# Optimization experiments

Hardware: AMD Instinct MI355X
Metric: run time of the kernel (lower is better)

## Reference

```python
import jax, jax.numpy as jnp
import numpy as np

EPS = 1e-9
N_NODES = 100000
N_EDGES = 1600000
N_FEAT = 256


def _normalize(x):
    # ProjectiveUHG.normalize: scale each point to the unit sphere (projective rep)
    return x / (jnp.linalg.norm(x, axis=-1, keepdims=True) + EPS)


def _mink(a, b):
    # UHG bilinear form: Euclidean on first d-1 coords, minus on the last
    return jnp.sum(a[..., :-1] * b[..., :-1], axis=-1) - a[..., -1] * b[..., -1]


def _uhg_dist(a, b):
    # projective quadrance q = 1 - <a,b>^2 / (<a,a><b,b>); distance = sqrt(q)
    q = 1.0 - _mink(a, b) ** 2 / (_mink(a, a) * _mink(b, b) + EPS)
    return jnp.sqrt(jnp.clip(q, 0.0))


def _message_pass(h, row, col):
    # vectorized gather -> per-edge UHG distance -> exp weight -> scatter-add
    xs = h[row]                                    # [E, D]
    xt = h[col]                                    # [E, D]
    w = jnp.exp(-_uhg_dist(xs, xt))[:, None]       # [E, 1]
    return jax.ops.segment_sum(xs * w, col, num_segments=h.shape[0])


def setup_inputs() -> dict:
    key = jax.random.key(0)
    ks = jax.random.split(key, 12)
    s = 0.05
    return {
        "x": jax.random.normal(ks[0], (N_NODES, N_FEAT), jnp.float32),
        "edge_index": jax.random.randint(ks[1], (2, N_EDGES), 0, N_NODES, jnp.int64 if jax.config.jax_enable_x64 else jnp.int32),
        "W_in": jax.random.normal(ks[2], (N_FEAT, 128), jnp.float32) * s,
        "b_in": jnp.zeros((128,), jnp.float32),
        "W1": jax.random.normal(ks[3], (128, 128), jnp.float32) * s,
        "b1": jnp.zeros((128,), jnp.float32),
        "W2": jax.random.normal(ks[4], (128, 64), jnp.float32) * s,
        "b2": jnp.zeros((64,), jnp.float32),
        "Wc1": jax.random.normal(ks[5], (64, 32), jnp.float32) * s,
        "bc1": jnp.zeros((32,), jnp.float32),
        "Wc2": jax.random.normal(ks[6], (32, 1), jnp.float32) * s,
        "bc2": jnp.zeros((1,), jnp.float32),
    }


def reference(x, edge_index, W_in, b_in, W1, b1, W2, b2, Wc1, bc1, Wc2, bc2):
    row, col = edge_index[0], edge_index[1]
    h = _normalize(jax.nn.relu(x @ W_in + b_in))       # [N, 128]
    agg = _message_pass(h, row, col)                   # [N, 128]
    h = _normalize(jax.nn.relu(agg @ W1 + b1))         # [N, 128]
    agg = _message_pass(h, row, col)                   # [N, 128]
    h = _normalize(jax.nn.relu(agg @ W2 + b2))         # [N, 64]
    h = jax.nn.relu(h @ Wc1 + bc1)                     # dropout is eval-mode identity
    return jax.nn.sigmoid(h @ Wc2 + bc2)               # [N, 1]
```

## Files before the change

### kernel.cpp

```cpp
#include <hip/hip_runtime.h>
#include <hip/hip_bf16.h>
#include <math.h>


template<int K, int M, bool WANT_MQ>
__global__ __launch_bounds__(256) void gemm_tile_norm(
    const float* __restrict__ A, const float* __restrict__ W,
    const float* __restrict__ bias, float* __restrict__ H,
    float* __restrict__ mqout, int N)
{
    constexpr int BM  = 128;
    constexpr int KB  = 32;
    constexpr int NTX = M / 8;
    constexpr int NTY = 256 / NTX;
    constexpr int TR  = BM / NTY;
    constexpr int SA  = BM + 4;
    constexpr int SW  = M + 4;

    __shared__ float As[KB][SA];
    __shared__ float Ws[KB][SW];

    const int tid  = threadIdx.x;
    const int tx   = tid % NTX;
    const int ty   = tid / NTX;
    const int row0 = blockIdx.x * BM;

    float acc[TR][8];
    #pragma unroll
    for (int r = 0; r < TR; ++r)
        #pragma unroll
        for (int c = 0; c < 8; ++c) acc[r][c] = 0.f;

    const int sf4 = tid % 8;
    const int sr0 = tid / 8;

    for (int kc = 0; kc < K / KB; ++kc) {
        if (kc) __syncthreads();
        #pragma unroll
        for (int t = 0; t < 4; ++t) {
            const int r    = t * 32 + sr0;
            const int grow = row0 + r;
            float4 v = {0.f, 0.f, 0.f, 0.f};
            if (grow < N)
                v = *(const float4*)(A + (size_t)grow * K + kc * KB + sf4 * 4);
            As[sf4 * 4 + 0][r] = v.x;
            As[sf4 * 4 + 1][r] = v.y;
            As[sf4 * 4 + 2][r] = v.z;
            As[sf4 * 4 + 3][r] = v.w;
        }
        #pragma unroll
        for (int t = 0; t < KB * M / 4 / 256; ++t) {
            const int idx = t * 256 + tid;
            const int kk  = idx / (M / 4);
            const int c4  = idx % (M / 4);
            *(float4*)&Ws[kk][c4 * 4] =
                *(const float4*)(W + (size_t)(kc * KB + kk) * M + c4 * 4);
        }
        __syncthreads();

        #pragma unroll 8
        for (int k = 0; k < KB; ++k) {
            const float4 w0 = *(const float4*)&Ws[k][tx * 8];
            const float4 w1 = *(const float4*)&Ws[k][tx * 8 + 4];
            float a[TR];
            #pragma unroll
            for (int rq = 0; rq < TR / 4; ++rq) {
                const float4 av = *(const float4*)&As[k][ty * TR + rq * 4];
                a[rq * 4 + 0] = av.x; a[rq * 4 + 1] = av.y;
                a[rq * 4 + 2] = av.z; a[rq * 4 + 3] = av.w;
            }
            #pragma unroll
            for (int r = 0; r < TR; ++r) {
                acc[r][0] += a[r] * w0.x;
                acc[r][1] += a[r] * w0.y;
                acc[r][2] += a[r] * w0.z;
                acc[r][3] += a[r] * w0.w;
                acc[r][4] += a[r] * w1.x;
                acc[r][5] += a[r] * w1.y;
                acc[r][6] += a[r] * w1.z;
                acc[r][7] += a[r] * w1.w;
            }
        }
    }

    const float4 b0 = *(const float4*)(bias + tx * 8);
    const float4 b1 = *(const float4*)(bias + tx * 8 + 4);

    #pragma unroll
    for (int r = 0; r < TR; ++r) {
        float v[8];
        v[0] = fmaxf(acc[r][0] + b0.x, 0.f);
        v[1] = fmaxf(acc[r][1] + b0.y, 0.f);
        v[2] = fmaxf(acc[r][2] + b0.z, 0.f);
        v[3] = fmaxf(acc[r][3] + b0.w, 0.f);
        v[4] = fmaxf(acc[r][4] + b1.x, 0.f);
        v[5] = fmaxf(acc[r][5] + b1.y, 0.f);
        v[6] = fmaxf(acc[r][6] + b1.z, 0.f);
        v[7] = fmaxf(acc[r][7] + b1.w, 0.f);

        float ss = 0.f;
        #pragma unroll
        for (int c = 0; c < 8; ++c) ss += v[c] * v[c];
        #pragma unroll
        for (int off = 1; off < NTX; off <<= 1) ss += __shfl_xor(ss, off);

        const float inv = 1.f / (sqrtf(ss) + 1e-9f);
        const int row = row0 + ty * TR + r;
        if (row < N) {
            float4 o0 = {v[0] * inv, v[1] * inv, v[2] * inv, v[3] * inv};
            float4 o1 = {v[4] * inv, v[5] * inv, v[6] * inv, v[7] * inv};
            *(float4*)(H + (size_t)row * M + tx * 8)     = o0;
            *(float4*)(H + (size_t)row * M + tx * 8 + 4) = o1;
            if (WANT_MQ && tx == NTX - 1) {
                const float hl = v[7] * inv;
                mqout[row] = ss * inv * inv - 2.f * hl * hl;
            }
        }
    }
}


__global__ void hist_kernel(const int* __restrict__ col, int* __restrict__ cnt, int E) {
    const int i = blockIdx.x * blockDim.x + threadIdx.x;
    if (i < E) atomicAdd(&cnt[col[i]], 1);
}

#define SCAN_TPB 256
#define SCAN_VPT 4

__global__ void scan1_kernel(const int* __restrict__ cnt, int* __restrict__ base,
                             int* __restrict__ bsum, int N) {
    __shared__ int s[SCAN_TPB];
    const int t  = threadIdx.x;
    const int i0 = blockIdx.x * (SCAN_TPB * SCAN_VPT) + t * SCAN_VPT;
    int v[SCAN_VPT]; int tot = 0;
    #pragma unroll
    for (int j = 0; j < SCAN_VPT; ++j) {
        v[j] = (i0 + j < N) ? cnt[i0 + j] : 0;
        tot += v[j];
    }
    s[t] = tot;
    __syncthreads();
    for (int off = 1; off < SCAN_TPB; off <<= 1) {
        const int x = (t >= off) ? s[t - off] : 0;
        __syncthreads();
        s[t] += x;
        __syncthreads();
    }
    const int excl = s[t] - tot;
    if (t == SCAN_TPB - 1) bsum[blockIdx.x] = s[SCAN_TPB - 1];
    int run = excl;
    #pragma unroll
    for (int j = 0; j < SCAN_VPT; ++j) {
        if (i0 + j < N) base[i0 + j] = run;
        run += v[j];
    }
}

__global__ void scan2_kernel(int* __restrict__ bsum, int nb) {
    __shared__ int s[SCAN_TPB];
    const int t = threadIdx.x;
    const int v = (t < nb) ? bsum[t] : 0;
    s[t] = v;
    __syncthreads();
    for (int off = 1; off < SCAN_TPB; off <<= 1) {
        const int x = (t >= off) ? s[t - off] : 0;
        __syncthreads();
        s[t] += x;
        __syncthreads();
    }
    if (t < nb) bsum[t] = s[t] - v;
}

__global__ void scan3_kernel(int* __restrict__ base, const int* __restrict__ bsum,
                             int* __restrict__ cursor, int N) {
    const int i = blockIdx.x * blockDim.x + threadIdx.x;
    if (i < N) {
        const int v = base[i] + bsum[i / (SCAN_TPB * SCAN_VPT)];
        base[i]   = v;
        cursor[i] = v;
    }
}

__global__ void scatter_kernel(const int* __restrict__ row, const int* __restrict__ col,
                               int* __restrict__ cursor, int* __restrict__ srow, int E) {
    const int i = blockIdx.x * blockDim.x + threadIdx.x;
    if (i < E) {
        const int pos = atomicAdd(&cursor[col[i]], 1);
        srow[pos] = row[i];
    }
}

__global__ __launch_bounds__(256) void message_pass_csr8(
    const float* __restrict__ h, const float* __restrict__ mq,
    const int* __restrict__ srow, const int* __restrict__ base,
    const int* __restrict__ cnt, float* __restrict__ agg, int N)
{
    const int node = (int)((blockIdx.x * 256u + threadIdx.x) >> 6);
    if (node >= N) return;
    const int lane = threadIdx.x & 63;
    const int gl   = lane & 7;
    const int g    = lane >> 3;

    const float4* hb = (const float4*)(h + (size_t)node * 128 + gl * 16);
    const float4 b0 = hb[0];
    const float4 b1 = hb[1];
    const float4 b2 = hb[2];
    const float4 b3 = hb[3];
    const float mqc = mq[node];

    const int nb = cnt[node];
    const int st = base[node];

    float4 acc0 = {0.f,0.f,0.f,0.f}, acc1 = {0.f,0.f,0.f,0.f};
    float4 acc2 = {0.f,0.f,0.f,0.f}, acc3 = {0.f,0.f,0.f,0.f};

    const int iters = (nb + 7) >> 3;
    for (int t = 0; t < iters; ++t) {
        const int ei  = t * 8 + g;
        const bool act = ei < nb;
        const int e   = st + (act ? ei : 0);
        const int r   = srow[e];
        const float4* ha = (const float4*)(h + (size_t)r * 128 + gl * 16);
        const float4 a0 = ha[0];
        const float4 a1 = ha[1];
        const float4 a2 = ha[2];
        const float4 a3 = ha[3];
        const float mqr = mq[r];

        float p = a0.x*b0.x + a0.y*b0.y + a0.z*b0.z + a0.w*b0.w
                + a1.x*b1.x + a1.y*b1.y + a1.z*b1.z + a1.w*b1.w
                + a2.x*b2.x + a2.y*b2.y + a2.z*b2.z + a2.w*b2.w
                + a3.x*b3.x + a3.y*b3.y + a3.z*b3.z;
        p += (gl == 7) ? -a3.w * b3.w : a3.w * b3.w;
        p += __shfl_xor(p, 1);
        p += __shfl_xor(p, 2);
        p += __shfl_xor(p, 4);

        const float denom = mqr * mqc + 1e-9f;
        float q = 1.f - (p * p) / denom;
        q = fmaxf(q, 0.f);
        float w = expf(-sqrtf(q));
        w = act ? w : 0.f;

        acc0.x += a0.x*w; acc0.y += a0.y*w; acc0.z += a0.z*w; acc0.w += a0.w*w;
        acc1.x += a1.x*w; acc1.y += a1.y*w; acc1.z += a1.z*w; acc1.w += a1.w*w;
        acc2.x += a2.x*w; acc2.y += a2.y*w; acc2.z += a2.z*w; acc2.w += a2.w*w;
        acc3.x += a3.x*w; acc3.y += a3.y*w; acc3.z += a3.z*w; acc3.w += a3.w*w;
    }

    #pragma unroll
    for (int off = 8; off < 64; off <<= 1) {
        acc0.x += __shfl_xor(acc0.x, off); acc0.y += __shfl_xor(acc0.y, off);
        acc0.z += __shfl_xor(acc0.z, off); acc0.w += __shfl_xor(acc0.w, off);
        acc1.x += __shfl_xor(acc1.x, off); acc1.y += __shfl_xor(acc1.y, off);
        acc1.z += __shfl_xor(acc1.z, off); acc1.w += __shfl_xor(acc1.w, off);
        acc2.x += __shfl_xor(acc2.x, off); acc2.y += __shfl_xor(acc2.y, off);
        acc2.z += __shfl_xor(acc2.z, off); acc2.w += __shfl_xor(acc2.w, off);
        acc3.x += __shfl_xor(acc3.x, off); acc3.y += __shfl_xor(acc3.y, off);
        acc3.z += __shfl_xor(acc3.z, off); acc3.w += __shfl_xor(acc3.w, off);
    }
    if (g == 0) {
        float4* out = (float4*)(agg + (size_t)node * 128 + gl * 16);
        out[0] = acc0;
        out[1] = acc1;
        out[2] = acc2;
        out[3] = acc3;
    }
}

__global__ __launch_bounds__(256) void message_pass(
    const float* __restrict__ h, const float* __restrict__ mq,
    const int* __restrict__ row, const int* __restrict__ col,
    float* __restrict__ agg, int E)
{
    const int wid  = (int)((blockIdx.x * (unsigned)blockDim.x + threadIdx.x) >> 6);
    const int lane = threadIdx.x & 63;
    if (wid >= E) return;

    const int r = row[wid];
    const int c = col[wid];

    const float a0 = h[(size_t)r * 128 + lane];
    const float a1 = h[(size_t)r * 128 + 64 + lane];
    const float b0 = h[(size_t)c * 128 + lane];
    const float b1 = h[(size_t)c * 128 + 64 + lane];

    float p = a0 * b0 + ((lane == 63) ? -a1 * b1 : a1 * b1);
    #pragma unroll
    for (int off = 1; off < 64; off <<= 1) p += __shfl_xor(p, off);

    const float denom = mq[r] * mq[c] + 1e-9f;
    float q = 1.f - (p * p) / denom;
    q = fmaxf(q, 0.f);
    const float w = expf(-sqrtf(q));

    atomicAdd(&agg[(size_t)c * 128 + lane],      a0 * w);
    atomicAdd(&agg[(size_t)c * 128 + 64 + lane], a1 * w);
}

__global__ __launch_bounds__(256) void classifier_kernel(
    const float* __restrict__ h3, const float* __restrict__ Wc1,
    const float* __restrict__ bc1, const float* __restrict__ Wc2,
    const float* __restrict__ bc2, float* __restrict__ out, int N)
{
    __shared__ float w1[64 * 32];
    __shared__ float w2[32];
    __shared__ float b1s[32];

    const int tid = threadIdx.x;
    for (int i = tid; i < 64 * 32; i += 256) w1[i] = Wc1[i];
    if (tid < 32) { w2[tid] = Wc2[tid]; b1s[tid] = bc1[tid]; }
    __syncthreads();

    const int n = blockIdx.x * 256 + tid;
    if (n >= N) return;

    float t1[32];
    #pragma unroll
    for (int c = 0; c < 32; ++c) t1[c] = b1s[c];

    const float4* hrow = (const float4*)(h3 + (size_t)n * 64);
    #pragma unroll
    for (int k4 = 0; k4 < 16; ++k4) {
        const float4 hv = hrow[k4];
        const int k = k4 * 4;
        #pragma unroll
        for (int c = 0; c < 32; ++c) {
            t1[c] += hv.x * w1[(k + 0) * 32 + c] + hv.y * w1[(k + 1) * 32 + c]
                   + hv.z * w1[(k + 2) * 32 + c] + hv.w * w1[(k + 3) * 32 + c];
        }
    }

    float z = bc2[0];
    #pragma unroll
    for (int c = 0; c < 32; ++c) z += fmaxf(t1[c], 0.f) * w2[c];
    out[n] = 1.f / (1.f + expf(-z));
}

extern "C" void kernel_launch(void* const* d_in, const int* in_sizes, int n_in,
                              void* d_out, int out_size, void* d_ws, size_t ws_size,
                              hipStream_t stream)
{
    const float* x    = (const float*)d_in[0];
    const int*   ei   = (const int*)  d_in[1];
    const float* W_in = (const float*)d_in[2];
    const float* b_in = (const float*)d_in[3];
    const float* W1   = (const float*)d_in[4];
    const float* b1   = (const float*)d_in[5];
    const float* W2   = (const float*)d_in[6];
    const float* b2   = (const float*)d_in[7];
    const float* Wc1  = (const float*)d_in[8];
    const float* bc1  = (const float*)d_in[9];
    const float* Wc2  = (const float*)d_in[10];
    const float* bc2  = (const float*)d_in[11];
    float* out = (float*)d_out;

    const int N = in_sizes[0] / 256;
    const int E = in_sizes[1] / 2;
    const int* row = ei;
    const int* col = ei + E;

    float* bufA = (float*)d_ws;
    float* bufB = bufA + (size_t)N * 128;
    float* mq   = bufB + (size_t)N * 128;
    int*   cnt  = (int*)(mq + N);
    int*   base = cnt + N;
    int*   cur  = base + N;
    int*   bsum = cur + N;
    int*   srow = bsum + 256;

    const size_t need = ((size_t)N * 257 + (size_t)N * 3 + 256 + (size_t)E) * 4;
    const bool use_csr = ws_size >= need;

    const int scan_blk = (N + SCAN_TPB * SCAN_VPT - 1) / (SCAN_TPB * SCAN_VPT);

    if (use_csr) {
        hipMemsetAsync(cnt, 0, (size_t)N * sizeof(int), stream);
        hist_kernel<<<(E + 255) / 256, 256, 0, stream>>>(col, cnt, E);
        scan1_kernel<<<scan_blk, SCAN_TPB, 0, stream>>>(cnt, base, bsum, N);
        scan2_kernel<<<1, SCAN_TPB, 0, stream>>>(bsum, scan_blk);
        scan3_kernel<<<(N + 255) / 256, 256, 0, stream>>>(base, bsum, cur, N);
        scatter_kernel<<<(E + 255) / 256, 256, 0, stream>>>(row, col, cur, srow, E);
    }

    const int gemm_blk = (N + 127) / 128;
    const int mp_blocks_csr = (N + 3) / 4;
    const int mp_blocks_atm = (E + 3) / 4;

    gemm_tile_norm<256, 128, true><<<gemm_blk, 256, 0, stream>>>(x, W_in, b_in, bufA, mq, N);
    if (use_csr) {
        message_pass_csr8<<<mp_blocks_csr, 256, 0, stream>>>(bufA, mq, srow, base, cnt, bufB, N);
    } else {
        hipMemsetAsync(bufB, 0, (size_t)N * 128 * sizeof(float), stream);
        message_pass<<<mp_blocks_atm, 256, 0, stream>>>(bufA, mq, row, col, bufB, E);
    }

    gemm_tile_norm<128, 128, true><<<gemm_blk, 256, 0, stream>>>(bufB, W1, b1, bufA, mq, N);
    if (use_csr) {
        message_pass_csr8<<<mp_blocks_csr, 256, 0, stream>>>(bufA, mq, srow, base, cnt, bufB, N);
    } else {
        hipMemsetAsync(bufB, 0, (size_t)N * 128 * sizeof(float), stream);
        message_pass<<<mp_blocks_atm, 256, 0, stream>>>(bufA, mq, row, col, bufB, E);
    }

    gemm_tile_norm<128, 64, false><<<gemm_blk, 256, 0, stream>>>(bufB, W2, b2, bufA, nullptr, N);

    classifier_kernel<<<(N + 255) / 256, 256, 0, stream>>>(bufA, Wc1, bc1, Wc2, bc2, out, N);
}
```

Before: 787.3 us.

## Presort edges by row then column buckets before CSR scatter

Replaces the single random atomic scatter that builds the CSR source list with a two-pass bucket sort: edges are first partitioned by source-row bucket, then stably by destination-column bucket, and only then scattered per destination. The goal is to make the final per-column scatter and the later gathers of source rows more local, so that neighbour lists are roughly ordered by source row and cache hits improve. The cost is two extra edge passes, extra bucket histograms and scans, and scratch arrays placed in bufA/bufB before those buffers are used. Bucket sizes are hardcoded to 512 buckets of 256 nodes, and atomic ordering inside a bucket is not stable.

```diff
diff --git a/kernel.cpp b/kernel.cpp
--- a/kernel.cpp
+++ b/kernel.cpp
@@ -125,6 +125,38 @@
     if (i < E) atomicAdd(&cnt[col[i]], 1);
 }
 
+__global__ void hist_buckets(const int* __restrict__ row, const int* __restrict__ col,
+                             int* __restrict__ rb, int* __restrict__ cb, int E, int nbk) {
+    __shared__ int hr[512];
+    __shared__ int hc[512];
+    for (int i = threadIdx.x; i < 512; i += blockDim.x) { hr[i] = 0; hc[i] = 0; }
+    __syncthreads();
+    for (int i = blockIdx.x * blockDim.x + threadIdx.x; i < E; i += gridDim.x * blockDim.x) {
+        atomicAdd(&hr[row[i] >> 8], 1);
+        atomicAdd(&hc[col[i] >> 8], 1);
+    }
+    __syncthreads();
+    for (int i = threadIdx.x; i < nbk; i += blockDim.x) {
+        if (hr[i]) atomicAdd(&rb[i], hr[i]);
+        if (hc[i]) atomicAdd(&cb[i], hc[i]);
+    }
+}
+
+__global__ void scan_small(int* __restrict__ data, int n) {
+    __shared__ int s[1024];
+    const int t = threadIdx.x;
+    const int v = (t < n) ? data[t] : 0;
+    s[t] = v;
+    __syncthreads();
+    for (int off = 1; off < 1024; off <<= 1) {
+        const int x = (t >= off) ? s[t - off] : 0;
+        __syncthreads();
+        s[t] += x;
+        __syncthreads();
+    }
+    if (t < n) data[t] = s[t] - v;
+}
+
 #define SCAN_TPB 256
 #define SCAN_VPT 4
 
@@ -182,12 +214,27 @@
     }
 }
 
-__global__ void scatter_kernel(const int* __restrict__ row, const int* __restrict__ col,
-                               int* __restrict__ cursor, int* __restrict__ srow, int E) {
+template<bool BYROW>
+__global__ void bucket_scatter(const int* __restrict__ rin, const int* __restrict__ cin,
+                               int* __restrict__ cursor,
+                               int* __restrict__ rout, int* __restrict__ cout, int E) {
     const int i = blockIdx.x * blockDim.x + threadIdx.x;
     if (i < E) {
-        const int pos = atomicAdd(&cursor[col[i]], 1);
-        srow[pos] = row[i];
+        const int r = rin[i], c = cin[i];
+        const int b = (BYROW ? r : c) >> 8;
+        const int pos = atomicAdd(&cursor[b], 1);
+        rout[pos] = r;
+        cout[pos] = c;
+    }
+}
+
+__global__ void final_scatter(const int* __restrict__ rin, const int* __restrict__ cin,
+                              int* __restrict__ cur, int* __restrict__ srow, int E) {
+    const int i = blockIdx.x * blockDim.x + threadIdx.x;
+    if (i < E) {
+        const int c = cin[i];
+        const int pos = atomicAdd(&cur[c], 1);
+        srow[pos] = rin[i];
     }
 }
 
@@ -370,18 +417,32 @@
     int*   bsum = cur + N;
     int*   srow = bsum + 256;
 
+    int* S    = (int*)bufA;
+    int* trr  = S + 1024;
+    int* trc  = trr + E;
+    int* t2r  = (int*)bufB;
+    int* t2c  = t2r + E;
+
     const size_t need = ((size_t)N * 257 + (size_t)N * 3 + 256 + (size_t)E) * 4;
     const bool use_csr = ws_size >= need;
 
     const int scan_blk = (N + SCAN_TPB * SCAN_VPT - 1) / (SCAN_TPB * SCAN_VPT);
+    const int NBK = (N + 255) >> 8;
+    const int eblk = (E + 255) / 256;
 
     if (use_csr) {
+        hipMemsetAsync(S, 0, 1024 * sizeof(int), stream);
         hipMemsetAsync(cnt, 0, (size_t)N * sizeof(int), stream);
-        hist_kernel<<<(E + 255) / 256, 256, 0, stream>>>(col, cnt, E);
+        hist_buckets<<<512, 256, 0, stream>>>(row, col, S, S + 512, E, NBK);
+        hist_kernel<<<eblk, 256, 0, stream>>>(col, cnt, E);
+        scan_small<<<1, 1024, 0, stream>>>(S, NBK);
+        scan_small<<<1, 1024, 0, stream>>>(S + 512, NBK);
         scan1_kernel<<<scan_blk, SCAN_TPB, 0, stream>>>(cnt, base, bsum, N);
         scan2_kernel<<<1, SCAN_TPB, 0, stream>>>(bsum, scan_blk);
         scan3_kernel<<<(N + 255) / 256, 256, 0, stream>>>(base, bsum, cur, N);
-        scatter_kernel<<<(E + 255) / 256, 256, 0, stream>>>(row, col, cur, srow, E);
+        bucket_scatter<true><<<eblk, 256, 0, stream>>>(row, col, S, trr, trc, E);
+        bucket_scatter<false><<<eblk, 256, 0, stream>>>(trr, trc, S + 512, t2r, t2c, E);
+        final_scatter<<<eblk, 256, 0, stream>>>(t2r, t2c, cur, srow, E);
     }
 
     const int gemm_blk = (N + 127) / 128;
```

Result: slower. 1.850 ms (+135.0%).
